# Kernel optimization log

Hardware: AMD Instinct MI355X
Metric: run time of the kernel (lower is better)

The kernel has to match this reference:

```python
import jax, jax.numpy as jnp
from jax import lax
import numpy as np

B, S, H, L = 128, 256, 768, 24


def setup_inputs() -> dict:
    key = jax.random.key(0)
    k_tf, k_len, k_w, k_tr, k_st, k_en = jax.random.split(key, 6)
    token_features = jax.random.normal(k_tf, (B, S, H), dtype=jnp.float32)
    # contiguous valid lengths in [3, S] (>=3 so that stripping CLS/SEP leaves >=1 token)
    lengths = jax.random.randint(k_len, (B,), 3, S + 1)
    pos = jnp.arange(S)
    input_mask = (pos[None, :] < lengths[:, None]).astype(jnp.int32)
    true_label_mask = (pos[None, :] < (lengths - 2)[:, None]).astype(jnp.int32)
    W = jax.random.normal(k_w, (H, L), dtype=jnp.float32) * 0.02
    b = jnp.zeros((L,), dtype=jnp.float32)
    transitions = jax.random.normal(k_tr, (L, L), dtype=jnp.float32) * 0.1
    start_trans = jax.random.normal(k_st, (L,), dtype=jnp.float32) * 0.1
    end_trans = jax.random.normal(k_en, (L,), dtype=jnp.float32) * 0.1
    return {
        "token_features": token_features,
        "input_mask": input_mask,
        "true_label_mask": true_label_mask,
        "W": W,
        "b": b,
        "transitions": transitions,
        "start_trans": start_trans,
        "end_trans": end_trans,
    }


def _compact(x, mask):
    """Vectorized version of the torch per-token copy loop: for each row,
    gather valid tokens (mask==1) preserving order, drop the first and last
    valid token (CLS/SEP), left-pack into a zero tensor."""
    # stable argsort puts valid positions first, in order
    order = jnp.argsort(1 - mask.astype(jnp.int32), axis=1)  # [B,S]
    gathered = jnp.take_along_axis(x, order[:, :, None], axis=1)  # [B,S,H]
    # drop first valid token (shift left by 1), pad a zero row at the end
    shifted = jnp.concatenate([gathered[:, 1:], jnp.zeros_like(gathered[:, :1])], axis=1)
    n_valid = mask.sum(axis=1)  # [B]
    keep = jnp.arange(x.shape[1])[None, :] < (n_valid[:, None] - 2)  # also drops last (SEP)
    return jnp.where(keep[:, :, None], shifted, 0.0)


def _viterbi(emissions, mask, transitions, start_trans, end_trans):
    """Masked Viterbi decode. emissions [B,S,L], mask [B,S] bool."""
    Bn, Sn, Ln = emissions.shape
    lbl = jnp.arange(Ln)
    score0 = start_trans[None, :] + emissions[:, 0]  # [B,L]

    def step(score, xs):
        em_t, m_t = xs  # [B,L], [B]
        cand = score[:, :, None] + transitions[None]  # [B,prev,curr]
        best = cand.max(axis=1) + em_t
        bp = cand.argmax(axis=1)  # [B,L] best prev tag per curr tag
        new_score = jnp.where(m_t[:, None], best, score)
        bp = jnp.where(m_t[:, None], bp, lbl[None, :])  # identity backpointer on pad
        return new_score, bp

    ems = jnp.swapaxes(emissions[:, 1:], 0, 1)  # [S-1,B,L]
    ms = jnp.swapaxes(mask[:, 1:], 0, 1)  # [S-1,B]
    final, bps = lax.scan(step, score0, (ems, ms))
    final = final + end_trans[None, :]
    best_score = final.max(axis=1)  # [B]
    last_tag = final.argmax(axis=1)  # [B]

    def back(tag, bp):  # tag: tag at time t; bp: bp_t -> tag at t-1
        prev = jnp.take_along_axis(bp, tag[:, None], axis=1)[:, 0]
        return prev, tag

    tag0, tags_rest = lax.scan(back, last_tag, bps, reverse=True)  # tags_rest [S-1,B]
    path = jnp.concatenate([tag0[:, None], jnp.swapaxes(tags_rest, 0, 1)], axis=1)  # [B,S]
    return best_score, path


def reference(token_features, input_mask, true_label_mask, W, b, transitions, start_trans, end_trans):
    mask = input_mask.astype(bool)
    wv = _compact(token_features, mask)  # dropout is identity at inference
    emissions = jax.nn.sigmoid(wv @ W + b)  # [B,S,L]
    _, path = _viterbi(emissions, true_label_mask != 0, transitions, start_trans, end_trans)
    return path
```

## Files before the change

kernel.cpp:

```cpp
#include <hip/hip_runtime.h>
#include <hip/hip_bf16.h>
#include <math.h>

#define NB 128
#define NS 256
#define NH 768
#define NL 24
#define ASTR 68

__global__ __launch_bounds__(256) void ner_emis(
    const float* __restrict__ tf, const int* __restrict__ tlm,
    const float* __restrict__ W, const float* __restrict__ bias,
    float* __restrict__ E)
{
    const int b    = blockIdx.x >> 3;
    const int tile = (blockIdx.x & 7) << 5;
    const int tid  = threadIdx.x;
    if (tlm[b*NS + tile] == 0) return;

    __shared__ float lds[8*32*25];
    float* As = lds;
    float* Ws = lds + 32*ASTR;
    float* Pr = lds;

    const int tok  = tid & 15;
    const int ksub = tid >> 4;
    const int kk   = ksub << 2;
    const int rot  = ksub & 3;

    float acc0[NL], acc1[NL];
    #pragma unroll
    for (int l = 0; l < NL; ++l) { acc0[l] = 0.f; acc1[l] = 0.f; }

    const float* tfb = tf + (size_t)(b*NS)*NH;

    for (int kc0 = 0; kc0 < NH; kc0 += 64) {
        #pragma unroll
        for (int i = 0; i < 2; ++i) {
            int idx  = tid + (i << 8);
            int row  = idx >> 4;
            int c4   = idx & 15;
            int trow = tile + row + 1;
            if (trow > 255) trow = 255;
            float4 v = *(const float4*)(tfb + (size_t)trow*NH + kc0 + (c4 << 2));
            float* dst = As + row*ASTR + (c4 << 2);
            dst[0] = v.x; dst[1] = v.y; dst[2] = v.z; dst[3] = v.w;
        }
        {
            const float4* wsrc = (const float4*)(W + (size_t)kc0*NL);
            float4* wdst = (float4*)Ws;
            for (int i = tid; i < 384; i += 256) wdst[i] = wsrc[i];
        }
        __syncthreads();

        const float* A0 = As + tok*ASTR + kk;
        const float* A1 = A0 + 16*ASTR;
        const float* Wr = Ws + kk*NL;
        #pragma unroll
        for (int s = 0; s < 4; ++s) {
            const int j = (s + rot) & 3;
            float a0 = A0[j];
            float a1 = A1[j];
            const float4* w4 = (const float4*)(Wr + j*NL);
            float wv[NL];
            #pragma unroll
            for (int i = 0; i < 6; ++i) {
                float4 w = w4[i];
                wv[4*i+0] = w.x; wv[4*i+1] = w.y; wv[4*i+2] = w.z; wv[4*i+3] = w.w;
            }
            #pragma unroll
            for (int l = 0; l < NL; ++l) {
                acc0[l] = fmaf(a0, wv[l], acc0[l]);
                acc1[l] = fmaf(a1, wv[l], acc1[l]);
            }
        }
        __syncthreads();
    }

    if (ksub >= 8) {
        float* p = Pr + ((ksub-8)*32 + tok)*25;
        float* q = p + 16*25;
        #pragma unroll
        for (int l = 0; l < NL; ++l) { p[l] = acc0[l]; q[l] = acc1[l]; }
    }
    __syncthreads();
    if (ksub < 8) {
        const float* p = Pr + (ksub*32 + tok)*25;
        const float* q = p + 16*25;
        #pragma unroll
        for (int l = 0; l < NL; ++l) { acc0[l] += p[l]; acc1[l] += q[l]; }
    }
    __syncthreads();
    if (ksub < 8) {
        float* p = Pr + (ksub*32 + tok)*25;
        float* q = p + 16*25;
        #pragma unroll
        for (int l = 0; l < NL; ++l) { p[l] = acc0[l]; q[l] = acc1[l]; }
    }
    __syncthreads();

    const int* tm = tlm + b*NS + tile;
    float* Eb = E + (size_t)(b*NS + tile)*NL;
    #pragma unroll
    for (int i = 0; i < 3; ++i) {
        int o = tid + (i << 8);
        int t = o / NL, l = o % NL;
        if (tm[t]) {
            float s = 0.f;
            #pragma unroll
            for (int ks = 0; ks < 8; ++ks)
                s += Pr[(ks*32 + t)*25 + l];
            float x = s + bias[l];
            Eb[t*NL + l] = 1.0f/(1.0f + expf(-x));
        }
    }
}

__global__ __launch_bounds__(256) void ner_viterbi(
    const float* __restrict__ E, const int* __restrict__ tlm,
    const float* __restrict__ trans, const float* __restrict__ st,
    const float* __restrict__ en, int* __restrict__ out)
{
    const int tid = threadIdx.x;
    const int b   = blockIdx.x;
    const int bS  = b*NS;

    __shared__ float Esh[NS*NL];
    __shared__ float scl[NS*NL];
    __shared__ float Tt[NL*NL];
    __shared__ float fin[NL];
    __shared__ unsigned char tr_s[NL][NS];
    __shared__ int chosen[12];
    __shared__ int nsh, ltag;

    {
        const float4* src = (const float4*)(E + (size_t)bS*NL);
        float4* dst = (float4*)Esh;
        #pragma unroll
        for (int j = 0; j < 6; ++j) dst[tid + (j << 8)] = src[tid + (j << 8)];
    }
    for (int i = tid; i < NL*NL; i += 256) {
        int c = i / NL, p = i % NL;
        Tt[i] = trans[p*NL + c];
    }
    if (tid < 64) {
        int a = tlm[bS+tid] + tlm[bS+tid+64] + tlm[bS+tid+128] + tlm[bS+tid+192];
        #pragma unroll
        for (int off = 32; off > 0; off >>= 1) a += __shfl_down(a, off, 64);
        if (tid == 0) nsh = a;
    }
    __syncthreads();
    const int n = nsh;

    if (tid < 64) {
        const int c = tid % 24;
        float Tc[24];
        #pragma unroll
        for (int p = 0; p < 24; ++p) Tc[p] = trans[p*NL + c];

        auto rl = [](float v, int p) {
            return __int_as_float(__builtin_amdgcn_readlane(__float_as_int(v), p));
        };

        float sv = st[c] + Esh[c];
        scl[c] = sv;
        float scr[24];
        #pragma unroll
        for (int p = 0; p < 24; ++p) scr[p] = rl(sv, p);

        auto step = [&](int t, float em) {
            float cand[24];
            #pragma unroll
            for (int p = 0; p < 24; ++p) cand[p] = scr[p] + Tc[p];
            float m0 = fmaxf(fmaxf(cand[0],  cand[1]),  cand[2]);
            float m1 = fmaxf(fmaxf(cand[3],  cand[4]),  cand[5]);
            float m2 = fmaxf(fmaxf(cand[6],  cand[7]),  cand[8]);
            float m3 = fmaxf(fmaxf(cand[9],  cand[10]), cand[11]);
            float m4 = fmaxf(fmaxf(cand[12], cand[13]), cand[14]);
            float m5 = fmaxf(fmaxf(cand[15], cand[16]), cand[17]);
            float m6 = fmaxf(fmaxf(cand[18], cand[19]), cand[20]);
            float m7 = fmaxf(fmaxf(cand[21], cand[22]), cand[23]);
            float q0 = fmaxf(fmaxf(m0, m1), m2);
            float q1 = fmaxf(fmaxf(m3, m4), m5);
            float q2 = fmaxf(m6, m7);
            float best = fmaxf(fmaxf(q0, q1), q2);
            sv = best + em;
            scl[t*NL + c] = sv;
            #pragma unroll
            for (int p = 0; p < 24; ++p) scr[p] = rl(sv, p);
        };

        int t = 1;
        for (; t + 8 <= n; t += 8) {
            float em[8];
            const float* eb = Esh + t*NL + c;
            #pragma unroll
            for (int j = 0; j < 8; ++j) em[j] = eb[j*NL];
            #pragma unroll
            for (int j = 0; j < 8; ++j) step(t + j, em[j]);
        }
        for (; t < n; ++t) step(t, Esh[t*NL + c]);
        fin[c] = sv + en[c];
    }
    __syncthreads();

    if (tid == 0) {
        float bv = fin[0]; int bt = 0;
        #pragma unroll
        for (int cc = 1; cc < 24; ++cc) { if (fin[cc] > bv) { bv = fin[cc]; bt = cc; } }
        ltag = bt;
    }
    __syncthreads();

    const int K = (n > 1) ? (n - 1 + 9) / 10 : 1;
    if (n > 1 && tid < 240) {
        const int w = tid / 24 + 1, h = tid % 24;
        int tlo = (w-1)*K; if (tlo > n-1) tlo = n-1;
        int thi = w*K;     if (thi > n-1) thi = n-1;
        int cur = h;
        for (int t = thi; t > tlo; --t) {
            const float4* sp = (const float4*)(scl + (t-1)*NL);
            const float4* up = (const float4*)(Tt  + cur*NL);
            float cand[24];
            #pragma unroll
            for (int i = 0; i < 6; ++i) {
                float4 s = sp[i], u = up[i];
                cand[4*i+0] = s.x + u.x;
                cand[4*i+1] = s.y + u.y;
                cand[4*i+2] = s.z + u.z;
                cand[4*i+3] = s.w + u.w;
            }
            float best = cand[0]; int arg = 0;
            #pragma unroll
            for (int p = 1; p < 24; ++p) { if (cand[p] > best) { best = cand[p]; arg = p; } }
            tr_s[h][t-1] = (unsigned char)arg;
            cur = arg;
        }
    }
    __syncthreads();

    if (tid == 0) {
        int cur = ltag;
        for (int w = 10; w >= 1; --w) {
            chosen[w] = cur;
            int tlo = (w-1)*K; if (tlo > n-1) tlo = n-1;
            int thi = w*K;     if (thi > n-1) thi = n-1;
            if (thi > tlo) cur = tr_s[cur][tlo];
        }
    }
    __syncthreads();

    {
        const int t = tid;
        int tag;
        if (t >= n-1) tag = ltag;
        else { int w = t / K + 1; tag = tr_s[chosen[w]][t]; }
        out[bS + t] = tag;
    }
}

extern "C" void kernel_launch(void* const* d_in, const int* in_sizes, int n_in,
                              void* d_out, int out_size, void* d_ws, size_t ws_size,
                              hipStream_t stream) {
    const float* tf    = (const float*)d_in[0];
    const int*   tlm   = (const int*)  d_in[2];
    const float* W     = (const float*)d_in[3];
    const float* bias  = (const float*)d_in[4];
    const float* trans = (const float*)d_in[5];
    const float* st    = (const float*)d_in[6];
    const float* en    = (const float*)d_in[7];
    float* E = (float*)d_ws;

    ner_emis<<<dim3(NB*8), dim3(256), 0, stream>>>(tf, tlm, W, bias, E);
    ner_viterbi<<<dim3(NB), dim3(256), 0, stream>>>(E, tlm, trans, st, en, (int*)d_out);
}
```

Before: 209.4 us.

## Fuse emission GEMM and Viterbi into one launch with per-batch ready counters

Merges the emission kernel and the Viterbi kernel into a single launch. The first NB blocks run Viterbi and spin on per-batch atomic counters, which the 8 emission tile blocks for that batch increment with release semantics when they finish. The Viterbi path now reads emissions straight from global memory with an 8-step register prefetch instead of staging them in LDS. This removes the second launch and its tail gap, and lets decoding of one batch overlap with emission work for others. In exchange it adds a memset, relies on all blocks becoming resident to avoid deadlock, and puts global-load latency on the serial Viterbi chain.

After: 254.8 us. +21.7%, slower.

```diff
diff --git a/kernel.cpp b/kernel.cpp
--- a/kernel.cpp
+++ b/kernel.cpp
@@ -1,5 +1,4 @@
 #include <hip/hip_runtime.h>
-#include <hip/hip_bf16.h>
 #include <math.h>
 
 #define NB 128
@@ -7,162 +6,173 @@
 #define NH 768
 #define NL 24
 #define ASTR 68
-
-__global__ __launch_bounds__(256) void ner_emis(
+#define E_BYTES (NB*NS*NL*4)
+
+__global__ __launch_bounds__(256) void ner_fused(
     const float* __restrict__ tf, const int* __restrict__ tlm,
     const float* __restrict__ W, const float* __restrict__ bias,
-    float* __restrict__ E)
+    const float* __restrict__ trans, const float* __restrict__ st,
+    const float* __restrict__ en, float* __restrict__ E,
+    int* __restrict__ ready, int* __restrict__ out)
 {
-    const int b    = blockIdx.x >> 3;
-    const int tile = (blockIdx.x & 7) << 5;
-    const int tid  = threadIdx.x;
-    if (tlm[b*NS + tile] == 0) return;
-
-    __shared__ float lds[8*32*25];
-    float* As = lds;
-    float* Ws = lds + 32*ASTR;
-    float* Pr = lds;
-
-    const int tok  = tid & 15;
-    const int ksub = tid >> 4;
-    const int kk   = ksub << 2;
-    const int rot  = ksub & 3;
-
-    float acc0[NL], acc1[NL];
-    #pragma unroll
-    for (int l = 0; l < NL; ++l) { acc0[l] = 0.f; acc1[l] = 0.f; }
-
-    const float* tfb = tf + (size_t)(b*NS)*NH;
-
-    for (int kc0 = 0; kc0 < NH; kc0 += 64) {
-        #pragma unroll
-        for (int i = 0; i < 2; ++i) {
-            int idx  = tid + (i << 8);
-            int row  = idx >> 4;
-            int c4   = idx & 15;
-            int trow = tile + row + 1;
-            if (trow > 255) trow = 255;
-            float4 v = *(const float4*)(tfb + (size_t)trow*NH + kc0 + (c4 << 2));
-            float* dst = As + row*ASTR + (c4 << 2);
-            dst[0] = v.x; dst[1] = v.y; dst[2] = v.z; dst[3] = v.w;
-        }
-        {
-            const float4* wsrc = (const float4*)(W + (size_t)kc0*NL);
-            float4* wdst = (float4*)Ws;
-            for (int i = tid; i < 384; i += 256) wdst[i] = wsrc[i];
+    __shared__ __align__(16) unsigned char smem[33184];
+    const int tid = threadIdx.x;
+
+    if (blockIdx.x >= NB) {
+        const int bid  = blockIdx.x - NB;
+        const int b    = bid >> 3;
+        const int tile = (bid & 7) << 5;
+        if (tlm[b*NS + tile] == 0) {
+            if (tid == 0)
+                __hip_atomic_fetch_add(&ready[b], 1, __ATOMIC_RELEASE, __HIP_MEMORY_SCOPE_AGENT);
+            return;
+        }
+
+        float* lds = (float*)smem;
+        float* As = lds;
+        float* Ws = lds + 32*ASTR;
+        float* Pr = lds;
+
+        const int tok  = tid & 15;
+        const int ksub = tid >> 4;
+        const int kk   = ksub << 2;
+        const int rot  = ksub & 3;
+
+        float acc0[NL], acc1[NL];
+        #pragma unroll
+        for (int l = 0; l < NL; ++l) { acc0[l] = 0.f; acc1[l] = 0.f; }
+
+        const float* tfb = tf + (size_t)(b*NS)*NH;
+
+        for (int kc0 = 0; kc0 < NH; kc0 += 64) {
+            #pragma unroll
+            for (int i = 0; i < 2; ++i) {
+                int idx  = tid + (i << 8);
+                int row  = idx >> 4;
+                int c4   = idx & 15;
+                int trow = tile + row + 1;
+                if (trow > 255) trow = 255;
+                float4 v = *(const float4*)(tfb + (size_t)trow*NH + kc0 + (c4 << 2));
+                float* dst = As + row*ASTR + (c4 << 2);
+                dst[0] = v.x; dst[1] = v.y; dst[2] = v.z; dst[3] = v.w;
+            }
+            {
+                const float4* wsrc = (const float4*)(W + (size_t)kc0*NL);
+                float4* wdst = (float4*)Ws;
+                for (int i = tid; i < 384; i += 256) wdst[i] = wsrc[i];
+            }
+            __syncthreads();
+
+            const float* A0 = As + tok*ASTR + kk;
+            const float* A1 = A0 + 16*ASTR;
+            const float* Wr = Ws + kk*NL;
+            #pragma unroll
+            for (int s = 0; s < 4; ++s) {
+                const int j = (s + rot) & 3;
+                float a0 = A0[j];
+                float a1 = A1[j];
+                const float4* w4 = (const float4*)(Wr + j*NL);
+                float wv[NL];
+                #pragma unroll
+                for (int i = 0; i < 6; ++i) {
+                    float4 w = w4[i];
+                    wv[4*i+0] = w.x; wv[4*i+1] = w.y; wv[4*i+2] = w.z; wv[4*i+3] = w.w;
+                }
+                #pragma unroll
+                for (int l = 0; l < NL; ++l) {
+                    acc0[l] = fmaf(a0, wv[l], acc0[l]);
+                    acc1[l] = fmaf(a1, wv[l], acc1[l]);
+                }
+            }
+            __syncthreads();
+        }
+
+        if (ksub >= 8) {
+            float* p = Pr + ((ksub-8)*32 + tok)*25;
+            float* q = p + 16*25;
+            #pragma unroll
+            for (int l = 0; l < NL; ++l) { p[l] = acc0[l]; q[l] = acc1[l]; }
         }
         __syncthreads();
-
-        const float* A0 = As + tok*ASTR + kk;
-        const float* A1 = A0 + 16*ASTR;
-        const float* Wr = Ws + kk*NL;
-        #pragma unroll
-        for (int s = 0; s < 4; ++s) {
-            const int j = (s + rot) & 3;
-            float a0 = A0[j];
-            float a1 = A1[j];
-            const float4* w4 = (const float4*)(Wr + j*NL);
-            float wv[NL];
-            #pragma unroll
-            for (int i = 0; i < 6; ++i) {
-                float4 w = w4[i];
-                wv[4*i+0] = w.x; wv[4*i+1] = w.y; wv[4*i+2] = w.z; wv[4*i+3] = w.w;
-            }
-            #pragma unroll
-            for (int l = 0; l < NL; ++l) {
-                acc0[l] = fmaf(a0, wv[l], acc0[l]);
-                acc1[l] = fmaf(a1, wv[l], acc1[l]);
-            }
+        if (ksub < 8) {
+            const float* p = Pr + (ksub*32 + tok)*25;
+            const float* q = p + 16*25;
+            #pragma unroll
+            for (int l = 0; l < NL; ++l) { acc0[l] += p[l]; acc1[l] += q[l]; }
         }
         __syncthreads();
-    }
-
-    if (ksub >= 8) {
-        float* p = Pr + ((ksub-8)*32 + tok)*25;
-        float* q = p + 16*25;
-        #pragma unroll
-        for (int l = 0; l < NL; ++l) { p[l] = acc0[l]; q[l] = acc1[l]; }
-    }
-    __syncthreads();
-    if (ksub < 8) {
-        const float* p = Pr + (ksub*32 + tok)*25;
-        const float* q = p + 16*25;
-        #pragma unroll
-        for (int l = 0; l < NL; ++l) { acc0[l] += p[l]; acc1[l] += q[l]; }
-    }
-    __syncthreads();
-    if (ksub < 8) {
-        float* p = Pr + (ksub*32 + tok)*25;
-        float* q = p + 16*25;
-        #pragma unroll
-        for (int l = 0; l < NL; ++l) { p[l] = acc0[l]; q[l] = acc1[l]; }
-    }
-    __syncthreads();
-
-    const int* tm = tlm + b*NS + tile;
-    float* Eb = E + (size_t)(b*NS + tile)*NL;
-    #pragma unroll
-    for (int i = 0; i < 3; ++i) {
-        int o = tid + (i << 8);
-        int t = o / NL, l = o % NL;
-        if (tm[t]) {
-            float s = 0.f;
-            #pragma unroll
-            for (int ks = 0; ks < 8; ++ks)
-                s += Pr[(ks*32 + t)*25 + l];
-            float x = s + bias[l];
-            Eb[t*NL + l] = 1.0f/(1.0f + expf(-x));
-        }
-    }
-}
-
-__global__ __launch_bounds__(256) void ner_viterbi(
-    const float* __restrict__ E, const int* __restrict__ tlm,
-    const float* __restrict__ trans, const float* __restrict__ st,
-    const float* __restrict__ en, int* __restrict__ out)
-{
-    const int tid = threadIdx.x;
-    const int b   = blockIdx.x;
-    const int bS  = b*NS;
-
-    __shared__ float Esh[NS*NL];
-    __shared__ float scl[NS*NL];
-    __shared__ float Tt[NL*NL];
-    __shared__ float fin[NL];
-    __shared__ unsigned char tr_s[NL][NS];
-    __shared__ int chosen[12];
-    __shared__ int nsh, ltag;
-
-    {
-        const float4* src = (const float4*)(E + (size_t)bS*NL);
-        float4* dst = (float4*)Esh;
-        #pragma unroll
-        for (int j = 0; j < 6; ++j) dst[tid + (j << 8)] = src[tid + (j << 8)];
-    }
-    for (int i = tid; i < NL*NL; i += 256) {
-        int c = i / NL, p = i % NL;
-        Tt[i] = trans[p*NL + c];
-    }
+        if (ksub < 8) {
+            float* p = Pr + (ksub*32 + tok)*25;
+            float* q = p + 16*25;
+            #pragma unroll
+            for (int l = 0; l < NL; ++l) { p[l] = acc0[l]; q[l] = acc1[l]; }
+        }
+        __syncthreads();
+
+        const int* tm = tlm + b*NS + tile;
+        float* Eb = E + (size_t)(b*NS + tile)*NL;
+        #pragma unroll
+        for (int i = 0; i < 3; ++i) {
+            int o = tid + (i << 8);
+            int t = o / NL, l = o % NL;
+            if (tm[t]) {
+                float s = 0.f;
+                #pragma unroll
+                for (int ks = 0; ks < 8; ++ks)
+                    s += Pr[(ks*32 + t)*25 + l];
+                float x = s + bias[l];
+                Eb[t*NL + l] = 1.0f/(1.0f + expf(-x));
+            }
+        }
+        __syncthreads();
+        if (tid == 0)
+            __hip_atomic_fetch_add(&ready[b], 1, __ATOMIC_RELEASE, __HIP_MEMORY_SCOPE_AGENT);
+        return;
+    }
+
+    const int b  = blockIdx.x;
+    const int bS = b*NS;
+
+    float* scl = (float*)smem;
+    float* Tt  = scl + NS*NL;
+    float* fin = Tt + NL*NL;
+    int*   chosen = (int*)(fin + NL);
+    int*   misc   = chosen + 12;
+    unsigned char* tr_s = (unsigned char*)(misc + 2);
+
+    const int c = tid % 24;
+    float Tc[24];
+
     if (tid < 64) {
+        #pragma unroll
+        for (int p = 0; p < 24; ++p) Tc[p] = trans[p*NL + c];
         int a = tlm[bS+tid] + tlm[bS+tid+64] + tlm[bS+tid+128] + tlm[bS+tid+192];
         #pragma unroll
         for (int off = 32; off > 0; off >>= 1) a += __shfl_down(a, off, 64);
-        if (tid == 0) nsh = a;
-    }
-    __syncthreads();
-    const int n = nsh;
+        if (tid == 0) misc[0] = a;
+    }
+    if (tid >= 64 && tid < 192) {
+        for (int i = tid - 64; i < NL*NL; i += 128) {
+            int cc = i / NL, p = i % NL;
+            Tt[i] = trans[p*NL + cc];
+        }
+    }
+    if (tid == 224) {
+        while (__hip_atomic_load(&ready[b], __ATOMIC_RELAXED, __HIP_MEMORY_SCOPE_AGENT) < 8)
+            __builtin_amdgcn_s_sleep(8);
+        __threadfence();
+    }
+    __syncthreads();
+    const int n = misc[0];
 
     if (tid < 64) {
-        const int c = tid % 24;
-        float Tc[24];
-        #pragma unroll
-        for (int p = 0; p < 24; ++p) Tc[p] = trans[p*NL + c];
+        const float* Eg = E + (size_t)bS*NL + c;
 
         auto rl = [](float v, int p) {
             return __int_as_float(__builtin_amdgcn_readlane(__float_as_int(v), p));
         };
 
-        float sv = st[c] + Esh[c];
+        float sv = st[c] + Eg[0];
         scl[c] = sv;
         float scr[24];
         #pragma unroll
@@ -190,16 +200,28 @@
             for (int p = 0; p < 24; ++p) scr[p] = rl(sv, p);
         };
 
+        float emA[8], emB[8];
+        #pragma unroll
+        for (int j = 0; j < 8; ++j) emA[j] = Eg[(size_t)(1+j)*NL];
+
         int t = 1;
         for (; t + 8 <= n; t += 8) {
-            float em[8];
-            const float* eb = Esh + t*NL + c;
-            #pragma unroll
-            for (int j = 0; j < 8; ++j) em[j] = eb[j*NL];
-            #pragma unroll
-            for (int j = 0; j < 8; ++j) step(t + j, em[j]);
-        }
-        for (; t < n; ++t) step(t, Esh[t*NL + c]);
+            #pragma unroll
+            for (int j = 0; j < 8; ++j) {
+                int r = t + 8 + j; if (r > 255) r = 255;
+                emB[j] = Eg[(size_t)r*NL];
+            }
+            #pragma unroll
+            for (int j = 0; j < 8; ++j) step(t + j, emA[j]);
+            #pragma unroll
+            for (int j = 0; j < 8; ++j) emA[j] = emB[j];
+        }
+        {
+            const int t0 = t;
+            #pragma unroll
+            for (int j = 0; j < 8; ++j)
+                if (t0 + j < n) step(t0 + j, emA[j]);
+        }
         fin[c] = sv + en[c];
     }
     __syncthreads();
@@ -208,9 +230,10 @@
         float bv = fin[0]; int bt = 0;
         #pragma unroll
         for (int cc = 1; cc < 24; ++cc) { if (fin[cc] > bv) { bv = fin[cc]; bt = cc; } }
-        ltag = bt;
-    }
-    __syncthreads();
+        misc[1] = bt;
+    }
+    __syncthreads();
+    const int ltag = misc[1];
 
     const int K = (n > 1) ? (n - 1 + 9) / 10 : 1;
     if (n > 1 && tid < 240) {
@@ -233,7 +256,7 @@
             float best = cand[0]; int arg = 0;
             #pragma unroll
             for (int p = 1; p < 24; ++p) { if (cand[p] > best) { best = cand[p]; arg = p; } }
-            tr_s[h][t-1] = (unsigned char)arg;
+            tr_s[h*NS + (t-1)] = (unsigned char)arg;
             cur = arg;
         }
     }
@@ -245,7 +268,7 @@
             chosen[w] = cur;
             int tlo = (w-1)*K; if (tlo > n-1) tlo = n-1;
             int thi = w*K;     if (thi > n-1) thi = n-1;
-            if (thi > tlo) cur = tr_s[cur][tlo];
+            if (thi > tlo) cur = tr_s[cur*NS + tlo];
         }
     }
     __syncthreads();
@@ -254,7 +277,7 @@
         const int t = tid;
         int tag;
         if (t >= n-1) tag = ltag;
-        else { int w = t / K + 1; tag = tr_s[chosen[w]][t]; }
+        else { int w = t / K + 1; tag = tr_s[chosen[w]*NS + t]; }
         out[bS + t] = tag;
     }
 }
@@ -269,8 +292,10 @@
     const float* trans = (const float*)d_in[5];
     const float* st    = (const float*)d_in[6];
     const float* en    = (const float*)d_in[7];
-    float* E = (float*)d_ws;
-
-    ner_emis<<<dim3(NB*8), dim3(256), 0, stream>>>(tf, tlm, W, bias, E);
-    ner_viterbi<<<dim3(NB), dim3(256), 0, stream>>>(E, tlm, trans, st, en, (int*)d_out);
+    float* E     = (float*)d_ws;
+    int*   ready = (int*)((char*)d_ws + E_BYTES);
+
+    hipMemsetAsync(ready, 0, NB*sizeof(int), stream);
+    ner_fused<<<dim3(NB + NB*8), dim3(256), 0, stream>>>(
+        tf, tlm, W, bias, trans, st, en, E, ready, (int*)d_out);
 }
```
